# Optimization experiments

Measured on AMD Instinct MI355X. Metric: run time of the kernel, lower is better.

The kernel has to match this reference:

```python
import jax, jax.numpy as jnp
import numpy as np

DIM = 128
NUM_NODE = 43097
B = 4096          # sessions / target nodes
L = 50            # items per session
N = B * L         # item nodes
E_INT = N * 4     # 'interacts' edges
ALPHA = 0.2       # LeakyReLU negative slope
MAX_POS = 200


def setup_inputs() -> dict:
    key = jax.random.key(0)
    ks = jax.random.split(key, 10)
    stdv = 1.0 / np.sqrt(DIM)
    u = lambda k, s: jax.random.uniform(k, s, jnp.float32, -stdv, stdv)
    emb = u(ks[0], (NUM_NODE, DIM))
    pos_emb = u(ks[1], (MAX_POS, DIM))
    target_emb = u(ks[2], (1, DIM))
    pi_w = u(ks[3], (DIM,))            # nn.Linear(dim, 1, bias=False)
    q_w = u(ks[4], (DIM, 2 * DIM))     # nn.Linear(2*dim, dim, bias=False)
    r_w = u(ks[5], (DIM, 2 * DIM))
    iid = jax.random.randint(ks[6], (N,), 0, NUM_NODE, jnp.int32)
    pid = jax.random.randint(ks[7], (N,), 0, MAX_POS, jnp.int32)
    tid = jnp.zeros((B,), jnp.int32)   # target_embedding has a single row
    int_src = jax.random.randint(ks[8], (E_INT,), 0, N, jnp.int32)
    int_dst = jax.random.randint(ks[9], (E_INT,), 0, N, jnp.int32)
    agg_src = jnp.arange(N, dtype=jnp.int32)                       # each item -> its target
    agg_dst = jnp.repeat(jnp.arange(B, dtype=jnp.int32), L)        # session id per item
    return dict(emb=emb, pos_emb=pos_emb, target_emb=target_emb, pi_w=pi_w,
                q_w=q_w, r_w=r_w, iid=iid, pid=pid, tid=tid,
                int_src=int_src, int_dst=int_dst, agg_src=agg_src, agg_dst=agg_dst)


def reference(emb, pos_emb, target_emb, pi_w, q_w, r_w,
              iid, pid, tid, int_src, int_dst, agg_src, agg_dst):
    h_n = emb[iid]          # [N, D] item features
    h_p = pos_emb[pid]      # [N, D] positional feature per 'agg' edge
    h_t = target_emb[tid]   # [B, D]

    # --- stage 1: 'interacts' subgraph -------------------------------------
    # e = leakyrelu(pi(u_mul_v)) computed without materializing [E, D] product twice
    logits = jnp.einsum('ed,ed->e', h_n[int_src] * pi_w, h_n[int_dst])  # [E_INT]
    logits = jax.nn.leaky_relu(logits, ALPHA)
    # edge_softmax over incoming edges of each destination (dropout = identity in eval)
    mx = jax.ops.segment_max(logits, int_dst, num_segments=N)
    ex = jnp.exp(logits - mx[int_dst])
    denom = jax.ops.segment_sum(ex, int_dst, num_segments=N)
    a = ex / denom[int_dst]                                             # [E_INT]
    ft = jax.ops.segment_sum(h_n[int_src] * a[:, None], int_dst, num_segments=N)  # [N, D]

    # --- stage 2: 'agg' subgraph (item -> target) ---------------------------
    edge_ft = ft[agg_src]                                               # [N, D] copy_src
    e2 = jnp.tanh(jnp.concatenate([edge_ft, h_p], axis=-1) @ q_w.T)     # [N, D]
    cnt = jax.ops.segment_sum(jnp.ones((agg_dst.shape[0],), jnp.float32), agg_dst, num_segments=B)
    mean = jax.ops.segment_sum(edge_ft, agg_dst, num_segments=B) / jnp.maximum(cnt, 1.0)[:, None]
    f = jnp.concatenate([h_t, mean], axis=-1) @ r_w.T                   # [B, D]
    # udf_agg: m = src_ft * <e, dst_ft>, then sum over incoming edges
    coef = jnp.sum(e2 * f[agg_dst], axis=-1, keepdims=True)             # [N, 1]
    select = jax.ops.segment_sum(edge_ft * coef, agg_dst, num_segments=B)  # [B, D]

    # scores against item embeddings [1:num_node]
    scores = select @ emb[1:NUM_NODE].T                                 # [B, NUM_NODE-1]
    return scores
```

## Files before the change

### kernel.cpp

```cpp
#include <hip/hip_runtime.h>

typedef unsigned short u16;
typedef unsigned int u32;
typedef float f32x4 __attribute__((ext_vector_type(4)));
typedef short short8 __attribute__((ext_vector_type(8)));

#define DIM 128
#define NUM_NODE 43097
#define NV (NUM_NODE - 1)
#define BB 4096
#define LL 50
#define NN (BB * LL)
#define EE (NN * 4)

__device__ __forceinline__ float b2f(u16 u) {
    union { u32 u; float f; } x; x.u = ((u32)u) << 16; return x.f;
}
__device__ __forceinline__ u16 f2b(float f) {
    union { float f; u32 u; } x; x.f = f;
    u32 r = x.u + 0x7FFFu + ((x.u >> 16) & 1u);
    return (u16)(r >> 16);
}

__global__ __launch_bounds__(256) void k_cvt(
    const float* __restrict__ s, u16* __restrict__ d, int n2)
{
    int i = blockIdx.x * 256 + threadIdx.x;
    if (i < n2) {
        float2 v = ((const float2*)s)[i];
        ((u32*)d)[i] = (u32)f2b(v.x) | ((u32)f2b(v.y) << 16);
    }
}

__global__ __launch_bounds__(256) void k_edge_logits(
    const u16* __restrict__ emb_bf, const float* __restrict__ pi_w,
    const int* __restrict__ iid, const int* __restrict__ int_src,
    const int* __restrict__ int_dst, float* __restrict__ logits,
    int* __restrict__ deg)
{
    int e = blockIdx.x * 4 + (threadIdx.x >> 6);
    int lane = threadIdx.x & 63;
    int s = int_src[e], d = int_dst[e];
    int sr = iid[s], dr = iid[d];
    ushort2 a = ((const ushort2*)(emb_bf + (size_t)sr * DIM))[lane];
    ushort2 b = ((const ushort2*)(emb_bf + (size_t)dr * DIM))[lane];
    float2 w = ((const float2*)pi_w)[lane];
    float part = b2f(a.x) * w.x * b2f(b.x) + b2f(a.y) * w.y * b2f(b.y);
    #pragma unroll
    for (int o = 32; o; o >>= 1) part += __shfl_xor(part, o, 64);
    if (lane == 0) {
        float lr = part >= 0.f ? part : 0.2f * part;
        logits[e] = lr;
        atomicAdd(&deg[d], 1);
    }
}

__global__ void k_block_sum(const int* __restrict__ deg, int* __restrict__ bsum)
{
    __shared__ int sm[256];
    int i = blockIdx.x * 256 + threadIdx.x;
    sm[threadIdx.x] = deg[i];
    __syncthreads();
    for (int s = 128; s > 0; s >>= 1) {
        if (threadIdx.x < s) sm[threadIdx.x] += sm[threadIdx.x + s];
        __syncthreads();
    }
    if (threadIdx.x == 0) bsum[blockIdx.x] = sm[0];
}

__global__ void k_scan_bsum(const int* __restrict__ bsum, int* __restrict__ boff)
{
    __shared__ int sm[1024];
    int t = threadIdx.x;
    int v = (t < 800) ? bsum[t] : 0;
    sm[t] = v;
    __syncthreads();
    for (int o = 1; o < 1024; o <<= 1) {
        int add = (t >= o) ? sm[t - o] : 0;
        __syncthreads();
        sm[t] += add;
        __syncthreads();
    }
    if (t < 800) boff[t] = sm[t] - v;
}

__global__ void k_scan_deg(const int* __restrict__ deg, const int* __restrict__ boff,
                           int* __restrict__ off)
{
    __shared__ int sm[256];
    int t = threadIdx.x;
    int i = blockIdx.x * 256 + t;
    int v = deg[i];
    sm[t] = v;
    __syncthreads();
    for (int o = 1; o < 256; o <<= 1) {
        int add = (t >= o) ? sm[t - o] : 0;
        __syncthreads();
        sm[t] += add;
        __syncthreads();
    }
    int incl = sm[t];
    int base = boff[blockIdx.x];
    off[i] = base + incl - v;
    if (i == NN - 1) off[NN] = base + incl;
}

__global__ void k_fill(const int* __restrict__ int_dst, const int* __restrict__ off,
                       int* __restrict__ cursor, int* __restrict__ e_sorted)
{
    int e = blockIdx.x * 256 + threadIdx.x;
    int d = int_dst[e];
    int slot = atomicAdd(&cursor[d], 1);
    e_sorted[off[d] + slot] = e;
}

__global__ __launch_bounds__(256) void k_softmax_ft(
    const u16* __restrict__ emb_bf, const int* __restrict__ iid,
    const int* __restrict__ int_src, const float* __restrict__ logits,
    const int* __restrict__ off, const int* __restrict__ e_sorted,
    u16* __restrict__ ft)
{
    int dst = blockIdx.x * 4 + (threadIdx.x >> 6);
    int lane = threadIdx.x & 63;
    int s0 = off[dst], s1 = off[dst + 1];
    u32* out = (u32*)(ft + (size_t)dst * DIM);
    if (s0 == s1) { out[lane] = 0u; return; }
    float m = -1e30f;
    for (int i = s0; i < s1; i++) m = fmaxf(m, logits[e_sorted[i]]);
    float ssum = 0.f, ax = 0.f, ay = 0.f;
    for (int i = s0; i < s1; i++) {
        int e = e_sorted[i];
        float w = __expf(logits[e] - m);
        ssum += w;
        int row = iid[int_src[e]];
        ushort2 u = ((const ushort2*)(emb_bf + (size_t)row * DIM))[lane];
        ax += w * b2f(u.x);
        ay += w * b2f(u.y);
    }
    float inv = 1.f / ssum;
    out[lane] = (u32)f2b(ax * inv) | ((u32)f2b(ay * inv) << 16);
}

__global__ __launch_bounds__(128) void k_mean_f(
    const u16* __restrict__ ft, const float* __restrict__ target_emb,
    const float* __restrict__ r_w, const int* __restrict__ tid,
    float* __restrict__ fmat)
{
    __shared__ float sht[DIM], smean[DIM];
    int b = blockIdx.x, t = threadIdx.x;
    size_t j0 = (size_t)b * LL;
    float s = 0.f;
    for (int i = 0; i < LL; i++) s += b2f(ft[(j0 + i) * DIM + t]);
    smean[t] = s * (1.f / (float)LL);
    sht[t] = target_emb[(size_t)tid[b] * DIM + t];
    __syncthreads();
    const float2* rw = (const float2*)(r_w + (size_t)t * 2 * DIM);
    float acc = 0.f;
    #pragma unroll 8
    for (int k = 0; k < 64; k++) {
        float2 u = rw[k];
        acc += sht[2 * k] * u.x + sht[2 * k + 1] * u.y;
    }
    #pragma unroll 8
    for (int k = 0; k < 64; k++) {
        float2 u = rw[64 + k];
        acc += smean[2 * k] * u.x + smean[2 * k + 1] * u.y;
    }
    fmat[(size_t)b * DIM + t] = acc;
}

#define K6_STRIDE 136
__global__ __launch_bounds__(256) void k_coef(
    const u16* __restrict__ ft, const u16* __restrict__ pos_bf,
    const u16* __restrict__ qw_bf, const int* __restrict__ pid,
    const int* __restrict__ agg_dst, const float* __restrict__ fmat,
    float* __restrict__ coef)
{
    extern __shared__ u16 smA[];
    int j0 = blockIdx.x * 128;
    int t = threadIdx.x;
    int wave = t >> 6, lane = t & 63, quad = lane >> 4, col = lane & 15;
    int m0 = wave * 32;

    f32x4 acc[2][8];
    #pragma unroll
    for (int mt = 0; mt < 2; mt++)
        #pragma unroll
        for (int nt = 0; nt < 8; nt++)
            acc[mt][nt] = (f32x4){0.f, 0.f, 0.f, 0.f};

    for (int h = 0; h < 2; h++) {
        __syncthreads();
        {
            int r = t >> 1;
            int j = j0 + r;
            const u16* src = h ? (pos_bf + (size_t)pid[j] * DIM)
                               : (ft + (size_t)j * DIM);
            const uint4* s4 = (const uint4*)src;
            uint4* d4 = (uint4*)(smA + r * K6_STRIDE);
            int c0 = (t & 1) * 8;
            #pragma unroll
            for (int c = 0; c < 8; c++) d4[c0 + c] = s4[c0 + c];
        }
        __syncthreads();
        #pragma unroll
        for (int kk = 0; kk < 4; kk++) {
            int koff = kk * 32 + quad * 8;
            short8 a0 = *(const short8*)(smA + (m0 + col) * K6_STRIDE + koff);
            short8 a1 = *(const short8*)(smA + (m0 + 16 + col) * K6_STRIDE + koff);
            #pragma unroll
            for (int nt = 0; nt < 8; nt++) {
                short8 b = *(const short8*)(qw_bf + (size_t)(nt * 16 + col) * 2 * DIM
                                            + h * DIM + koff);
                acc[0][nt] = __builtin_amdgcn_mfma_f32_16x16x32_bf16(a0, b, acc[0][nt], 0, 0, 0);
                acc[1][nt] = __builtin_amdgcn_mfma_f32_16x16x32_bf16(a1, b, acc[1][nt], 0, 0, 0);
            }
        }
    }

    #pragma unroll
    for (int mt = 0; mt < 2; mt++) {
        float part[4];
        #pragma unroll
        for (int reg = 0; reg < 4; reg++) {
            int jrow = j0 + m0 + mt * 16 + quad * 4 + reg;
            int sess = agg_dst[jrow];
            const float* fr = fmat + (size_t)sess * DIM;
            float p = 0.f;
            #pragma unroll
            for (int nt = 0; nt < 8; nt++) {
                float x = acc[mt][nt][reg];
                x = fminf(fmaxf(x, -15.f), 15.f);
                float e2x = __expf(2.f * x);
                float th = (e2x - 1.f) / (e2x + 1.f);
                p += th * fr[nt * 16 + col];
            }
            part[reg] = p;
        }
        #pragma unroll
        for (int o = 1; o < 16; o <<= 1)
            #pragma unroll
            for (int reg = 0; reg < 4; reg++)
                part[reg] += __shfl_xor(part[reg], o, 64);
        if (col == 0) {
            #pragma unroll
            for (int reg = 0; reg < 4; reg++)
                coef[j0 + m0 + mt * 16 + quad * 4 + reg] = part[reg];
        }
    }
}

__global__ __launch_bounds__(128) void k_select(
    const u16* __restrict__ ft, const float* __restrict__ coef,
    u16* __restrict__ selectb)
{
    int b = blockIdx.x, t = threadIdx.x;
    size_t j0 = (size_t)b * LL;
    float s = 0.f;
    for (int i = 0; i < LL; i++) {
        size_t j = j0 + i;
        s += coef[j] * b2f(ft[j * DIM + t]);
    }
    selectb[(size_t)b * DIM + t] = f2b(s);
}

#define K8_STRIDE 136
__global__ __launch_bounds__(256) void k_scores(
    const u16* __restrict__ selectb, const u16* __restrict__ emb_bf,
    float* __restrict__ out)
{
    extern __shared__ u16 sm[];
    int n0 = blockIdx.x * 128;
    int m0v = blockIdx.y * 128;
    int t = threadIdx.x;
    {
        int r = t >> 1;
        const uint4* s4 = (const uint4*)(selectb + (size_t)(m0v + r) * DIM);
        uint4* d4 = (uint4*)(sm + r * K8_STRIDE);
        int c0 = (t & 1) * 8;
        #pragma unroll
        for (int c = 0; c < 8; c++) d4[c0 + c] = s4[c0 + c];
    }
    __syncthreads();
    int wave = t >> 6, lane = t & 63, quad = lane >> 4, col = lane & 15;
    int m0 = wave * 32;
    f32x4 acc[2][8];
    #pragma unroll
    for (int mt = 0; mt < 2; mt++)
        #pragma unroll
        for (int nt = 0; nt < 8; nt++)
            acc[mt][nt] = (f32x4){0.f, 0.f, 0.f, 0.f};

    #pragma unroll
    for (int kk = 0; kk < 4; kk++) {
        int koff = kk * 32 + quad * 8;
        short8 a0 = *(const short8*)(sm + (m0 + col) * K8_STRIDE + koff);
        short8 a1 = *(const short8*)(sm + (m0 + 16 + col) * K8_STRIDE + koff);
        #pragma unroll
        for (int nt = 0; nt < 8; nt++) {
            int v = n0 + nt * 16 + col;
            int er = v + 1;
            if (er > NV) er = NV;
            short8 b = *(const short8*)(emb_bf + (size_t)er * DIM + koff);
            acc[0][nt] = __builtin_amdgcn_mfma_f32_16x16x32_bf16(a0, b, acc[0][nt], 0, 0, 0);
            acc[1][nt] = __builtin_amdgcn_mfma_f32_16x16x32_bf16(a1, b, acc[1][nt], 0, 0, 0);
        }
    }
    #pragma unroll
    for (int mt = 0; mt < 2; mt++)
        #pragma unroll
        for (int reg = 0; reg < 4; reg++) {
            int row = m0v + m0 + mt * 16 + quad * 4 + reg;
            float* orow = out + (size_t)row * NV;
            #pragma unroll
            for (int nt = 0; nt < 8; nt++) {
                int v = n0 + nt * 16 + col;
                if (v < NV) orow[v] = acc[mt][nt][reg];
            }
        }
}

extern "C" void kernel_launch(void* const* d_in, const int* in_sizes, int n_in,
                              void* d_out, int out_size, void* d_ws, size_t ws_size,
                              hipStream_t stream)
{
    const float* emb        = (const float*)d_in[0];
    const float* pos_emb    = (const float*)d_in[1];
    const float* target_emb = (const float*)d_in[2];
    const float* pi_w       = (const float*)d_in[3];
    const float* q_w        = (const float*)d_in[4];
    const float* r_w        = (const float*)d_in[5];
    const int* iid          = (const int*)d_in[6];
    const int* pid          = (const int*)d_in[7];
    const int* tid          = (const int*)d_in[8];
    const int* int_src      = (const int*)d_in[9];
    const int* int_dst      = (const int*)d_in[10];
    const int* agg_dst      = (const int*)d_in[12];
    float* out = (float*)d_out;

    char* ws = (char*)d_ws;
    u16*   emb_bf  = (u16*)  (ws + 0);
    u16*   pos_bf  = (u16*)  (ws + 11032832);
    u16*   qw_bf   = (u16*)  (ws + 11084032);
    float* logits  = (float*)(ws + 11149568);
    int*   deg     = (int*)  (ws + 14426368);
    int*   off     = (int*)  (ws + 15245568);
    int*   cursor  = (int*)  (ws + 16065024);
    int*   bsum    = (int*)  (ws + 16884224);
    int*   boff    = (int*)  (ws + 16887424);
    int*   e_sorted= (int*)  (ws + 16890880);
    u16*   ft      = (u16*)  (ws + 20167680);
    float* fmat    = (float*)(ws + 72596480);
    float* coef    = (float*)(ws + 74693632);
    u16*   selectb = (u16*)  (ws + 75512832);

    hipMemsetAsync(deg, 0, NN * sizeof(int), stream);
    hipMemsetAsync(cursor, 0, NN * sizeof(int), stream);

    k_cvt<<<(NUM_NODE * DIM / 2 + 255) / 256, 256, 0, stream>>>(emb, emb_bf, NUM_NODE * DIM / 2);
    k_cvt<<<(200 * DIM / 2 + 255) / 256, 256, 0, stream>>>(pos_emb, pos_bf, 200 * DIM / 2);
    k_cvt<<<(DIM * 2 * DIM / 2 + 255) / 256, 256, 0, stream>>>(q_w, qw_bf, DIM * 2 * DIM / 2);

    k_edge_logits<<<EE / 4, 256, 0, stream>>>(emb_bf, pi_w, iid, int_src, int_dst, logits, deg);
    k_block_sum<<<NN / 256, 256, 0, stream>>>(deg, bsum);
    k_scan_bsum<<<1, 1024, 0, stream>>>(bsum, boff);
    k_scan_deg<<<NN / 256, 256, 0, stream>>>(deg, boff, off);
    k_fill<<<EE / 256, 256, 0, stream>>>(int_dst, off, cursor, e_sorted);
    k_softmax_ft<<<NN / 4, 256, 0, stream>>>(emb_bf, iid, int_src, logits, off, e_sorted, ft);
    k_mean_f<<<BB, 128, 0, stream>>>(ft, target_emb, r_w, tid, fmat);
    k_coef<<<NN / 128, 256, 128 * K6_STRIDE * 2, stream>>>(ft, pos_bf, qw_bf, pid, agg_dst, fmat, coef);
    k_select<<<BB, 128, 0, stream>>>(ft, coef, selectb);
    dim3 g8((NV + 127) / 128, BB / 128);
    k_scores<<<g8, 256, 128 * K8_STRIDE * 2, stream>>>(selectb, emb_bf, out);
}
```

Baseline: 1.516 ms.

## Use 32x32 MFMA, vectorize gather kernels, swap scores grid order

Edge-logit and softmax kernels now give each edge or destination 16 lanes with 16-byte vector loads instead of a full wave with 4-byte loads. k_coef and k_scores switch from 16x16x32 to 32x32x16 bf16 MFMA, read A operands straight from global memory instead of staging them in LDS, and k_scores swaps its grid order so consecutive blocks share emb columns and writes output with nontemporal stores. The mean and select reductions read packed bf16 pairs split across two waves. This aims to cut memory-instruction count and LDS sync overhead, at the cost of more register pressure and possibly less reuse of A from cache.

```diff
diff --git a/kernel.cpp b/kernel.cpp
--- a/kernel.cpp
+++ b/kernel.cpp
@@ -3,6 +3,7 @@
 typedef unsigned short u16;
 typedef unsigned int u32;
 typedef float f32x4 __attribute__((ext_vector_type(4)));
+typedef float f32x16 __attribute__((ext_vector_type(16)));
 typedef short short8 __attribute__((ext_vector_type(8)));
 
 #define DIM 128
@@ -38,17 +39,23 @@
     const int* __restrict__ int_dst, float* __restrict__ logits,
     int* __restrict__ deg)
 {
-    int e = blockIdx.x * 4 + (threadIdx.x >> 6);
-    int lane = threadIdx.x & 63;
+    int t = threadIdx.x;
+    int e = blockIdx.x * 16 + (t >> 4);
+    int i = t & 15;
     int s = int_src[e], d = int_dst[e];
     int sr = iid[s], dr = iid[d];
-    ushort2 a = ((const ushort2*)(emb_bf + (size_t)sr * DIM))[lane];
-    ushort2 b = ((const ushort2*)(emb_bf + (size_t)dr * DIM))[lane];
-    float2 w = ((const float2*)pi_w)[lane];
-    float part = b2f(a.x) * w.x * b2f(b.x) + b2f(a.y) * w.y * b2f(b.y);
-    #pragma unroll
-    for (int o = 32; o; o >>= 1) part += __shfl_xor(part, o, 64);
-    if (lane == 0) {
+    uint4 ua = ((const uint4*)(emb_bf + (size_t)sr * DIM))[i];
+    uint4 ub = ((const uint4*)(emb_bf + (size_t)dr * DIM))[i];
+    const float4* p4 = (const float4*)pi_w;
+    float4 w0 = p4[i * 2], w1 = p4[i * 2 + 1];
+    float part =
+        b2f((u16)ua.x) * w0.x * b2f((u16)ub.x) + b2f((u16)(ua.x >> 16)) * w0.y * b2f((u16)(ub.x >> 16)) +
+        b2f((u16)ua.y) * w0.z * b2f((u16)ub.y) + b2f((u16)(ua.y >> 16)) * w0.w * b2f((u16)(ub.y >> 16)) +
+        b2f((u16)ua.z) * w1.x * b2f((u16)ub.z) + b2f((u16)(ua.z >> 16)) * w1.y * b2f((u16)(ub.z >> 16)) +
+        b2f((u16)ua.w) * w1.z * b2f((u16)ub.w) + b2f((u16)(ua.w >> 16)) * w1.w * b2f((u16)(ub.w >> 16));
+    #pragma unroll
+    for (int o = 1; o < 16; o <<= 1) part += __shfl_xor(part, o, 64);
+    if (i == 0) {
         float lr = part >= 0.f ? part : 0.2f * part;
         logits[e] = lr;
         atomicAdd(&deg[d], 1);
@@ -120,25 +127,34 @@
     const int* __restrict__ off, const int* __restrict__ e_sorted,
     u16* __restrict__ ft)
 {
-    int dst = blockIdx.x * 4 + (threadIdx.x >> 6);
-    int lane = threadIdx.x & 63;
+    int t = threadIdx.x;
+    int dst = blockIdx.x * 16 + (t >> 4);
+    int i = t & 15;
     int s0 = off[dst], s1 = off[dst + 1];
-    u32* out = (u32*)(ft + (size_t)dst * DIM);
-    if (s0 == s1) { out[lane] = 0u; return; }
+    uint4* outp = (uint4*)(ft + (size_t)dst * DIM);
+    if (s0 == s1) { outp[i] = (uint4){0u, 0u, 0u, 0u}; return; }
     float m = -1e30f;
-    for (int i = s0; i < s1; i++) m = fmaxf(m, logits[e_sorted[i]]);
-    float ssum = 0.f, ax = 0.f, ay = 0.f;
-    for (int i = s0; i < s1; i++) {
-        int e = e_sorted[i];
+    for (int k = s0; k < s1; k++) m = fmaxf(m, logits[e_sorted[k]]);
+    float a0 = 0.f, a1 = 0.f, a2 = 0.f, a3 = 0.f;
+    float a4 = 0.f, a5 = 0.f, a6 = 0.f, a7 = 0.f, ssum = 0.f;
+    for (int k = s0; k < s1; k++) {
+        int e = e_sorted[k];
         float w = __expf(logits[e] - m);
         ssum += w;
         int row = iid[int_src[e]];
-        ushort2 u = ((const ushort2*)(emb_bf + (size_t)row * DIM))[lane];
-        ax += w * b2f(u.x);
-        ay += w * b2f(u.y);
+        uint4 u = ((const uint4*)(emb_bf + (size_t)row * DIM))[i];
+        a0 += w * b2f((u16)u.x); a1 += w * b2f((u16)(u.x >> 16));
+        a2 += w * b2f((u16)u.y); a3 += w * b2f((u16)(u.y >> 16));
+        a4 += w * b2f((u16)u.z); a5 += w * b2f((u16)(u.z >> 16));
+        a6 += w * b2f((u16)u.w); a7 += w * b2f((u16)(u.w >> 16));
     }
     float inv = 1.f / ssum;
-    out[lane] = (u32)f2b(ax * inv) | ((u32)f2b(ay * inv) << 16);
+    uint4 r;
+    r.x = (u32)f2b(a0 * inv) | ((u32)f2b(a1 * inv) << 16);
+    r.y = (u32)f2b(a2 * inv) | ((u32)f2b(a3 * inv) << 16);
+    r.z = (u32)f2b(a4 * inv) | ((u32)f2b(a5 * inv) << 16);
+    r.w = (u32)f2b(a6 * inv) | ((u32)f2b(a7 * inv) << 16);
+    outp[i] = r;
 }
 
 __global__ __launch_bounds__(128) void k_mean_f(
@@ -147,12 +163,19 @@
     float* __restrict__ fmat)
 {
     __shared__ float sht[DIM], smean[DIM];
+    __shared__ float part[2][DIM];
     int b = blockIdx.x, t = threadIdx.x;
+    int w = t >> 6, c = t & 63;
     size_t j0 = (size_t)b * LL;
-    float s = 0.f;
-    for (int i = 0; i < LL; i++) s += b2f(ft[(j0 + i) * DIM + t]);
-    smean[t] = s * (1.f / (float)LL);
+    float sx = 0.f, sy = 0.f;
+    for (int i = w; i < LL; i += 2) {
+        u32 v = ((const u32*)(ft + (j0 + i) * DIM))[c];
+        sx += b2f((u16)v); sy += b2f((u16)(v >> 16));
+    }
+    part[w][2 * c] = sx; part[w][2 * c + 1] = sy;
     sht[t] = target_emb[(size_t)tid[b] * DIM + t];
+    __syncthreads();
+    smean[t] = (part[0][t] + part[1][t]) * (1.f / (float)LL);
     __syncthreads();
     const float2* rw = (const float2*)(r_w + (size_t)t * 2 * DIM);
     float acc = 0.f;
@@ -169,84 +192,68 @@
     fmat[(size_t)b * DIM + t] = acc;
 }
 
-#define K6_STRIDE 136
 __global__ __launch_bounds__(256) void k_coef(
     const u16* __restrict__ ft, const u16* __restrict__ pos_bf,
     const u16* __restrict__ qw_bf, const int* __restrict__ pid,
     const int* __restrict__ agg_dst, const float* __restrict__ fmat,
     float* __restrict__ coef)
 {
-    extern __shared__ u16 smA[];
     int j0 = blockIdx.x * 128;
     int t = threadIdx.x;
-    int wave = t >> 6, lane = t & 63, quad = lane >> 4, col = lane & 15;
+    int wave = t >> 6, lane = t & 63;
+    int l31 = lane & 31, half = lane >> 5;
     int m0 = wave * 32;
-
-    f32x4 acc[2][8];
-    #pragma unroll
-    for (int mt = 0; mt < 2; mt++)
-        #pragma unroll
-        for (int nt = 0; nt < 8; nt++)
-            acc[mt][nt] = (f32x4){0.f, 0.f, 0.f, 0.f};
-
+    int myrow = j0 + m0 + l31;
+    const u16* aft  = ft + (size_t)myrow * DIM;
+    const u16* apos = pos_bf + (size_t)pid[myrow] * DIM;
+
+    f32x16 acc[4];
+    #pragma unroll
+    for (int nt = 0; nt < 4; nt++)
+        #pragma unroll
+        for (int q = 0; q < 16; q++) acc[nt][q] = 0.f;
+
+    #pragma unroll
     for (int h = 0; h < 2; h++) {
-        __syncthreads();
-        {
-            int r = t >> 1;
-            int j = j0 + r;
-            const u16* src = h ? (pos_bf + (size_t)pid[j] * DIM)
-                               : (ft + (size_t)j * DIM);
-            const uint4* s4 = (const uint4*)src;
-            uint4* d4 = (uint4*)(smA + r * K6_STRIDE);
-            int c0 = (t & 1) * 8;
+        const u16* arow = h ? apos : aft;
+        #pragma unroll
+        for (int ks = 0; ks < 8; ks++) {
+            short8 a = *(const short8*)(arow + ks * 16 + half * 8);
             #pragma unroll
-            for (int c = 0; c < 8; c++) d4[c0 + c] = s4[c0 + c];
-        }
-        __syncthreads();
-        #pragma unroll
-        for (int kk = 0; kk < 4; kk++) {
-            int koff = kk * 32 + quad * 8;
-            short8 a0 = *(const short8*)(smA + (m0 + col) * K6_STRIDE + koff);
-            short8 a1 = *(const short8*)(smA + (m0 + 16 + col) * K6_STRIDE + koff);
-            #pragma unroll
-            for (int nt = 0; nt < 8; nt++) {
-                short8 b = *(const short8*)(qw_bf + (size_t)(nt * 16 + col) * 2 * DIM
-                                            + h * DIM + koff);
-                acc[0][nt] = __builtin_amdgcn_mfma_f32_16x16x32_bf16(a0, b, acc[0][nt], 0, 0, 0);
-                acc[1][nt] = __builtin_amdgcn_mfma_f32_16x16x32_bf16(a1, b, acc[1][nt], 0, 0, 0);
+            for (int nt = 0; nt < 4; nt++) {
+                short8 b = *(const short8*)(qw_bf + (size_t)(nt * 32 + l31) * (2 * DIM)
+                                            + h * DIM + ks * 16 + half * 8);
+                acc[nt] = __builtin_amdgcn_mfma_f32_32x32x16_bf16(a, b, acc[nt], 0, 0, 0);
             }
         }
     }
 
-    #pragma unroll
-    for (int mt = 0; mt < 2; mt++) {
-        float part[4];
-        #pragma unroll
-        for (int reg = 0; reg < 4; reg++) {
-            int jrow = j0 + m0 + mt * 16 + quad * 4 + reg;
-            int sess = agg_dst[jrow];
-            const float* fr = fmat + (size_t)sess * DIM;
-            float p = 0.f;
-            #pragma unroll
-            for (int nt = 0; nt < 8; nt++) {
-                float x = acc[mt][nt][reg];
-                x = fminf(fmaxf(x, -15.f), 15.f);
-                float e2x = __expf(2.f * x);
-                float th = (e2x - 1.f) / (e2x + 1.f);
-                p += th * fr[nt * 16 + col];
-            }
-            part[reg] = p;
+    float p[16];
+    #pragma unroll
+    for (int reg = 0; reg < 16; reg++) {
+        int j = j0 + m0 + (reg & 3) + 8 * (reg >> 2) + 4 * half;
+        int sess = agg_dst[j];
+        const float* fr = fmat + (size_t)sess * DIM;
+        float s = 0.f;
+        #pragma unroll
+        for (int nt = 0; nt < 4; nt++) {
+            float x = acc[nt][reg];
+            x = fminf(fmaxf(x, -15.f), 15.f);
+            float e2x = __expf(2.f * x);
+            float th = (e2x - 1.f) / (e2x + 1.f);
+            s += th * fr[nt * 32 + l31];
         }
-        #pragma unroll
-        for (int o = 1; o < 16; o <<= 1)
-            #pragma unroll
-            for (int reg = 0; reg < 4; reg++)
-                part[reg] += __shfl_xor(part[reg], o, 64);
-        if (col == 0) {
-            #pragma unroll
-            for (int reg = 0; reg < 4; reg++)
-                coef[j0 + m0 + mt * 16 + quad * 4 + reg] = part[reg];
-        }
+        p[reg] = s;
+    }
+    #pragma unroll
+    for (int o = 1; o < 32; o <<= 1)
+        #pragma unroll
+        for (int reg = 0; reg < 16; reg++)
+            p[reg] += __shfl_xor(p[reg], o, 64);
+    if (l31 == 0) {
+        #pragma unroll
+        for (int reg = 0; reg < 16; reg++)
+            coef[j0 + m0 + (reg & 3) + 8 * (reg >> 2) + 4 * half] = p[reg];
     }
 }
 
@@ -254,70 +261,65 @@
     const u16* __restrict__ ft, const float* __restrict__ coef,
     u16* __restrict__ selectb)
 {
+    __shared__ float part[2][DIM];
     int b = blockIdx.x, t = threadIdx.x;
+    int w = t >> 6, c = t & 63;
     size_t j0 = (size_t)b * LL;
-    float s = 0.f;
-    for (int i = 0; i < LL; i++) {
+    float sx = 0.f, sy = 0.f;
+    for (int i = w; i < LL; i += 2) {
         size_t j = j0 + i;
-        s += coef[j] * b2f(ft[j * DIM + t]);
-    }
-    selectb[(size_t)b * DIM + t] = f2b(s);
-}
-
-#define K8_STRIDE 136
+        float cf = coef[j];
+        u32 v = ((const u32*)(ft + j * DIM))[c];
+        sx += cf * b2f((u16)v); sy += cf * b2f((u16)(v >> 16));
+    }
+    part[w][2 * c] = sx; part[w][2 * c + 1] = sy;
+    __syncthreads();
+    if (t < 64) {
+        float x0 = part[0][2 * t] + part[1][2 * t];
+        float x1 = part[0][2 * t + 1] + part[1][2 * t + 1];
+        ((u32*)(selectb + (size_t)b * DIM))[t] = (u32)f2b(x0) | ((u32)f2b(x1) << 16);
+    }
+}
+
 __global__ __launch_bounds__(256) void k_scores(
     const u16* __restrict__ selectb, const u16* __restrict__ emb_bf,
     float* __restrict__ out)
 {
-    extern __shared__ u16 sm[];
-    int n0 = blockIdx.x * 128;
-    int m0v = blockIdx.y * 128;
-    int t = threadIdx.x;
-    {
-        int r = t >> 1;
-        const uint4* s4 = (const uint4*)(selectb + (size_t)(m0v + r) * DIM);
-        uint4* d4 = (uint4*)(sm + r * K8_STRIDE);
-        int c0 = (t & 1) * 8;
-        #pragma unroll
-        for (int c = 0; c < 8; c++) d4[c0 + c] = s4[c0 + c];
-    }
-    __syncthreads();
-    int wave = t >> 6, lane = t & 63, quad = lane >> 4, col = lane & 15;
-    int m0 = wave * 32;
-    f32x4 acc[2][8];
-    #pragma unroll
-    for (int mt = 0; mt < 2; mt++)
-        #pragma unroll
-        for (int nt = 0; nt < 8; nt++)
-            acc[mt][nt] = (f32x4){0.f, 0.f, 0.f, 0.f};
-
-    #pragma unroll
-    for (int kk = 0; kk < 4; kk++) {
-        int koff = kk * 32 + quad * 8;
-        short8 a0 = *(const short8*)(sm + (m0 + col) * K8_STRIDE + koff);
-        short8 a1 = *(const short8*)(sm + (m0 + 16 + col) * K8_STRIDE + koff);
-        #pragma unroll
-        for (int nt = 0; nt < 8; nt++) {
-            int v = n0 + nt * 16 + col;
+    int m0v = blockIdx.x * 128;
+    int n0  = blockIdx.y * 128;
+    int t = threadIdx.x;
+    int wave = t >> 6, lane = t & 63;
+    int l31 = lane & 31, half = lane >> 5;
+    const u16* A = selectb + (size_t)(m0v + wave * 32 + l31) * DIM;
+
+    f32x16 acc[4];
+    #pragma unroll
+    for (int nt = 0; nt < 4; nt++)
+        #pragma unroll
+        for (int q = 0; q < 16; q++) acc[nt][q] = 0.f;
+
+    #pragma unroll
+    for (int ks = 0; ks < 8; ks++) {
+        short8 a = *(const short8*)(A + ks * 16 + half * 8);
+        #pragma unroll
+        for (int nt = 0; nt < 4; nt++) {
+            int v = n0 + nt * 32 + l31;
             int er = v + 1;
             if (er > NV) er = NV;
-            short8 b = *(const short8*)(emb_bf + (size_t)er * DIM + koff);
-            acc[0][nt] = __builtin_amdgcn_mfma_f32_16x16x32_bf16(a0, b, acc[0][nt], 0, 0, 0);
-            acc[1][nt] = __builtin_amdgcn_mfma_f32_16x16x32_bf16(a1, b, acc[1][nt], 0, 0, 0);
+            short8 b = *(const short8*)(emb_bf + (size_t)er * DIM + ks * 16 + half * 8);
+            acc[nt] = __builtin_amdgcn_mfma_f32_32x32x16_bf16(a, b, acc[nt], 0, 0, 0);
         }
     }
     #pragma unroll
-    for (int mt = 0; mt < 2; mt++)
-        #pragma unroll
-        for (int reg = 0; reg < 4; reg++) {
-            int row = m0v + m0 + mt * 16 + quad * 4 + reg;
-            float* orow = out + (size_t)row * NV;
-            #pragma unroll
-            for (int nt = 0; nt < 8; nt++) {
-                int v = n0 + nt * 16 + col;
-                if (v < NV) orow[v] = acc[mt][nt][reg];
-            }
+    for (int reg = 0; reg < 16; reg++) {
+        int row = m0v + wave * 32 + (reg & 3) + 8 * (reg >> 2) + 4 * half;
+        float* orow = out + (size_t)row * NV;
+        #pragma unroll
+        for (int nt = 0; nt < 4; nt++) {
+            int v = n0 + nt * 32 + l31;
+            if (v < NV) __builtin_nontemporal_store(acc[nt][reg], &orow[v]);
         }
+    }
 }
 
 extern "C" void kernel_launch(void* const* d_in, const int* in_sizes, int n_in,
@@ -361,15 +363,15 @@
     k_cvt<<<(200 * DIM / 2 + 255) / 256, 256, 0, stream>>>(pos_emb, pos_bf, 200 * DIM / 2);
     k_cvt<<<(DIM * 2 * DIM / 2 + 255) / 256, 256, 0, stream>>>(q_w, qw_bf, DIM * 2 * DIM / 2);
 
-    k_edge_logits<<<EE / 4, 256, 0, stream>>>(emb_bf, pi_w, iid, int_src, int_dst, logits, deg);
+    k_edge_logits<<<EE / 16, 256, 0, stream>>>(emb_bf, pi_w, iid, int_src, int_dst, logits, deg);
     k_block_sum<<<NN / 256, 256, 0, stream>>>(deg, bsum);
     k_scan_bsum<<<1, 1024, 0, stream>>>(bsum, boff);
     k_scan_deg<<<NN / 256, 256, 0, stream>>>(deg, boff, off);
     k_fill<<<EE / 256, 256, 0, stream>>>(int_dst, off, cursor, e_sorted);
-    k_softmax_ft<<<NN / 4, 256, 0, stream>>>(emb_bf, iid, int_src, logits, off, e_sorted, ft);
+    k_softmax_ft<<<NN / 16, 256, 0, stream>>>(emb_bf, iid, int_src, logits, off, e_sorted, ft);
     k_mean_f<<<BB, 128, 0, stream>>>(ft, target_emb, r_w, tid, fmat);
-    k_coef<<<NN / 128, 256, 128 * K6_STRIDE * 2, stream>>>(ft, pos_bf, qw_bf, pid, agg_dst, fmat, coef);
+    k_coef<<<NN / 128, 256, 0, stream>>>(ft, pos_bf, qw_bf, pid, agg_dst, fmat, coef);
     k_select<<<BB, 128, 0, stream>>>(ft, coef, selectb);
-    dim3 g8((NV + 127) / 128, BB / 128);
-    k_scores<<<g8, 256, 128 * K8_STRIDE * 2, stream>>>(selectb, emb_bf, out);
-}
+    dim3 g8(BB / 128, (NV + 127) / 128);
+    k_scores<<<g8, 256, 0, stream>>>(selectb, emb_bf, out);
+}
```

Measured after the change: 1.250 ms. 1.21x faster.
